# Optimization experiments

Hardware: AMD Instinct MI355X
Metric: run time of the kernel (lower is better)

## Reference

```python
import jax, jax.numpy as jnp
import numpy as np

B, S, D, H = 4, 2048, 1024, 16
HD = D // H
EPS = 1e-7  # K.epsilon()


def setup_inputs() -> dict:
    key = jax.random.key(0)
    ks = jax.random.split(key, 5)
    scale = 1.0 / np.sqrt(D)  # keep projections numerically tame (glorot-ish)
    return {
        "x": jax.random.normal(ks[0], (B, S, D), dtype=jnp.float32),
        "Wq": jax.random.normal(ks[1], (D, D), dtype=jnp.float32) * scale,
        "bq": jnp.zeros((D,), dtype=jnp.float32),
        "Wk": jax.random.normal(ks[2], (D, D), dtype=jnp.float32) * scale,
        "bk": jnp.zeros((D,), dtype=jnp.float32),
        "Wv": jax.random.normal(ks[3], (D, D), dtype=jnp.float32) * scale,
        "bv": jnp.zeros((D,), dtype=jnp.float32),
        "Wo": jax.random.normal(ks[4], (D, D), dtype=jnp.float32) * scale,
        "bo": jnp.zeros((D,), dtype=jnp.float32),
    }


def _split_heads(t):
    # [B,S,D] -> [B,H,S,HD]
    return t.reshape(B, S, H, HD).transpose(0, 2, 1, 3)


def reference(x, Wq, bq, Wk, bk, Wv, bv, Wo, bo):
    relu = jax.nn.relu
    # projections with post-activation (keras layer applies activation to each mapping)
    q = _split_heads(relu(x @ Wq + bq))
    k = _split_heads(relu(x @ Wk + bk))
    v = _split_heads(relu(x @ Wv + bv))
    # scaled dot-product scores, scale = sqrt(head_dim)
    e = jnp.einsum("bhqd,bhkd->bhqk", q, k) / jnp.sqrt(jnp.asarray(HD, x.dtype))
    # exp with row max over ALL keys (before masking), as in the source
    e = jnp.exp(e - jnp.max(e, axis=-1, keepdims=True))
    # history_only: multiplicative causal mask applied AFTER exp
    causal = (jnp.arange(S)[None, :] <= jnp.arange(S)[:, None]).astype(x.dtype)
    e = e * causal  # broadcasts over [B,H,S,S]
    a = e / (jnp.sum(e, axis=-1, keepdims=True) + EPS)
    ctx = jnp.einsum("bhqk,bhkd->bhqd", a, v)
    y = ctx.transpose(0, 2, 1, 3).reshape(B, S, D)  # merge heads
    return relu(y @ Wo + bo)
```

## Files before the change

kernel.cpp:

```cpp
#include <hip/hip_runtime.h>
#include <hip/hip_bf16.h>
#include <cstdint>
#include <cstddef>

#define B_  4
#define S_  2048
#define D_  1024
#define H_  16
#define HD_ 64

typedef _Float16 half8  __attribute__((ext_vector_type(8)));
typedef _Float16 half4v __attribute__((ext_vector_type(4)));
typedef float    f32x4  __attribute__((ext_vector_type(4)));

__device__ __forceinline__ void async_copy16(const void* g, void* l) {
    __builtin_amdgcn_global_load_lds(
        (const __attribute__((address_space(1))) unsigned int*)g,
        (__attribute__((address_space(3))) unsigned int*)l,
        16, 0, 0);
}

__device__ __forceinline__ half8 hscale8(half8 v, _Float16 s) {
    #pragma unroll
    for (int i = 0; i < 8; ++i) v[i] *= s;
    return v;
}


__global__ void cast_x_kernel(const float4* __restrict__ in, half4v* __restrict__ out, int n4) {
    int i = blockIdx.x * 256 + threadIdx.x;
    if (i < n4) {
        float4 v = in[i];
        half4v h = { (_Float16)v.x, (_Float16)v.y, (_Float16)v.z, (_Float16)v.w };
        out[i] = h;
    }
}

__global__ void transpose_cast4_kernel(
    const float* __restrict__ W0, const float* __restrict__ W1,
    const float* __restrict__ W2, const float* __restrict__ W3,
    _Float16* __restrict__ T0, _Float16* __restrict__ T1,
    _Float16* __restrict__ T2, _Float16* __restrict__ T3)
{
    __shared__ float tile[32][33];
    const float* Wsel[4] = { W0, W1, W2, W3 };
    _Float16*    Tsel[4] = { T0, T1, T2, T3 };
    const float* W  = Wsel[blockIdx.z];
    _Float16*    Wt = Tsel[blockIdx.z];
    const int bn = blockIdx.x * 32, bk = blockIdx.y * 32;
    const int tx = threadIdx.x, ty = threadIdx.y;
    #pragma unroll
    for (int i = 0; i < 32; i += 8)
        tile[ty + i][tx] = W[(size_t)(bk + ty + i) * D_ + bn + tx];
    __syncthreads();
    #pragma unroll
    for (int i = 0; i < 32; i += 8)
        Wt[(size_t)(bn + ty + i) * D_ + bk + tx] = (_Float16)tile[tx][ty + i];
}

template<int OUT_MODE>
__global__ __launch_bounds__(256, 2) void gemm_bt_kernel(
    const _Float16* __restrict__ A, const _Float16* __restrict__ Bt,
    const float* __restrict__ b0, const float* __restrict__ b1,
    const float* __restrict__ b2,
    void* __restrict__ C0, void* __restrict__ C1, void* __restrict__ C2,
    int M, int N, int K)
{
    __shared__ _Float16 As[128 * 64];
    __shared__ _Float16 Bs[128 * 64];
    const int tid  = threadIdx.x;
    const int wid  = tid >> 6, lane = tid & 63;
    const int lr   = lane & 15, lq = lane >> 4;
    const int m0   = blockIdx.x * 128, n0 = blockIdx.y * 128;
    const int wm   = (wid >> 1) * 64, wn = (wid & 1) * 64;
    const int srow = tid >> 3;
    const int csw  = ((tid & 7) ^ (srow & 7)) * 8;

    f32x4 acc[4][4] = {};

    for (int k0 = 0; k0 < K; k0 += 64) {
        __syncthreads();
        #pragma unroll
        for (int i = 0; i < 4; ++i) {
            async_copy16(A  + (size_t)(m0 + i * 32 + srow) * K + k0 + csw,
                         (char*)As + (i * 256 + wid * 64) * 16);
            async_copy16(Bt + (size_t)(n0 + i * 32 + srow) * K + k0 + csw,
                         (char*)Bs + (i * 256 + wid * 64) * 16);
        }
        __syncthreads();
        #pragma unroll
        for (int ks = 0; ks < 2; ++ks) {
            half8 af[4], bf[4];
            #pragma unroll
            for (int t = 0; t < 4; ++t) {
                af[t] = *(const half8*)(As + (wm + t * 16 + lr) * 64 + (((ks * 4 + lq) ^ (lr & 7)) * 8));
                bf[t] = *(const half8*)(Bs + (wn + t * 16 + lr) * 64 + (((ks * 4 + lq) ^ (lr & 7)) * 8));
            }
            #pragma unroll
            for (int mt = 0; mt < 4; ++mt)
                #pragma unroll
                for (int nt = 0; nt < 4; ++nt)
                    acc[mt][nt] = __builtin_amdgcn_mfma_f32_16x16x32_f16(
                        af[mt], bf[nt], acc[mt][nt], 0, 0, 0);
        }
    }

    const int seg = (OUT_MODE == 3) ? (n0 >> 10) : 0;
    const float* bp = (OUT_MODE == 3) ? (seg == 0 ? b0 : (seg == 1 ? b1 : b2)) : b0;

    #pragma unroll
    for (int mt = 0; mt < 4; ++mt) {
        const int row = m0 + wm + mt * 16 + lq * 4;
        #pragma unroll
        for (int nt = 0; nt < 4; ++nt) {
            const int col = n0 + wn + nt * 16 + lr;
            const int cl  = (OUT_MODE == 3) ? (col & 1023) : col;
            const float bb = bp[cl];
            if (OUT_MODE == 3 && seg == 2) {
                const int b = row >> 11, sq = row & 2047;
                const int h = cl >> 6, hd = cl & 63;
                half4v o;
                #pragma unroll
                for (int r = 0; r < 4; ++r) {
                    float v = acc[mt][nt][r] + bb;
                    o[r] = (_Float16)(v > 0.0f ? v : 0.0f);
                }
                *(half4v*)((_Float16*)C2 +
                           ((size_t)(b * 16 + h) * 64 + hd) * S_ + sq) = o;
            } else if (OUT_MODE == 3) {
                _Float16* dst = (_Float16*)(seg ? C1 : C0);
                #pragma unroll
                for (int r = 0; r < 4; ++r) {
                    float v = acc[mt][nt][r] + bb;
                    dst[(size_t)(row + r) * 1024 + cl] = (_Float16)(v > 0.0f ? v : 0.0f);
                }
            } else {
                #pragma unroll
                for (int r = 0; r < 4; ++r) {
                    float v = acc[mt][nt][r] + bb;
                    ((float*)C0)[(size_t)(row + r) * N + col] = v > 0.0f ? v : 0.0f;
                }
            }
        }
    }
}

__global__ __launch_bounds__(256, 4) void attn_kernel(
    const _Float16* __restrict__ Qg, const _Float16* __restrict__ Kg,
    const _Float16* __restrict__ Vtg, _Float16* __restrict__ Y)
{
    __shared__ _Float16 Ks[2][64 * 64];
    __shared__ _Float16 Vt[2][64 * 64];
    __shared__ _Float16 Ps[4][16 * 64];

    const int qt_lo = blockIdx.x;
    const int qt_hi = 31 - qt_lo;
    const int bh = blockIdx.y;
    const int b  = bh >> 4, h = bh & 15;
    const int tid = threadIdx.x, wid = tid >> 6, lane = tid & 63;
    const int lr = lane & 15, lq = lane >> 4;

    const size_t base  = ((size_t)b * S_) * D_ + (size_t)h * HD_;
    const _Float16* Vh = Vtg + (size_t)bh * 64 * S_;

    const int srow = tid >> 3;
    const int csw  = ((tid & 7) ^ (srow & 7)) * 8;

    const int qts[2] = { qt_lo, qt_hi };
    half8 aq[2][2];
    #pragma unroll
    for (int s = 0; s < 2; ++s) {
        const _Float16* qp = Qg + base + (size_t)(qts[s] * 64 + wid * 16 + lr) * D_;
        aq[s][0] = hscale8(*(const half8*)(qp + lq * 8),      (_Float16)0.18033688f);
        aq[s][1] = hscale8(*(const half8*)(qp + 32 + lq * 8), (_Float16)0.18033688f);
    }

    float lsum[2] = { 0.0f, 0.0f };
    f32x4 O[2][4] = {};

    auto issue_tile = [&](int kb) {
        const int bufi = kb & 1;
        #pragma unroll
        for (int i = 0; i < 2; ++i) {
            async_copy16(Kg + base + (size_t)(kb * 64 + i * 32 + srow) * D_ + csw,
                         (char*)Ks[bufi] + (i * 256 + wid * 64) * 16);
            async_copy16(Vh + (size_t)(i * 32 + srow) * S_ + kb * 64 + csw,
                         (char*)Vt[bufi] + (i * 256 + wid * 64) * 16);
        }
    };

    issue_tile(0);

    for (int kb = 0; kb <= qt_hi; ++kb) {
        const int cur = kb & 1;
        __syncthreads();
        if (kb < qt_hi) issue_tile(kb + 1);

        const _Float16* Kc = Ks[cur];
        const _Float16* Vc = Vt[cur];

        #pragma unroll
        for (int s = 0; s < 2; ++s) {
            if (s == 0 && kb > qt_lo) continue;

            f32x4 sc[4] = {};
            #pragma unroll
            for (int ks = 0; ks < 2; ++ks) {
                half8 kf[4];
                #pragma unroll
                for (int t = 0; t < 4; ++t)
                    kf[t] = *(const half8*)(Kc + (t * 16 + lr) * 64 + (((ks * 4 + lq) ^ (lr & 7)) * 8));
                #pragma unroll
                for (int t = 0; t < 4; ++t)
                    sc[t] = __builtin_amdgcn_mfma_f32_16x16x32_f16(kf[t], aq[s][ks], sc[t], 0, 0, 0);
            }

            const bool diag = (kb == qts[s]);
            const int qg = qts[s] * 64 + wid * 16 + lr;
            const int kbase = kb * 64 + lq * 4;
            float sum = 0.0f;
            _Float16* pw = Ps[wid];
            #pragma unroll
            for (int t = 0; t < 4; ++t) {
                half4v pv;
                #pragma unroll
                for (int r = 0; r < 4; ++r) {
                    float ev = __builtin_amdgcn_exp2f(fminf(sc[t][r] - 5.770780f, 15.8696f));
                    if (diag)
                        ev = (kbase + t * 16 + r <= qg) ? ev : 0.0f;
                    pv[r] = (_Float16)ev;
                    sum += ev;
                }
                *(half4v*)(pw + lr * 64 + (((t * 2 + (lq >> 1)) ^ (lr & 7)) * 8) + (lq & 1) * 4) = pv;
            }
            lsum[s] += sum;

            asm volatile("s_waitcnt lgkmcnt(0)" ::: "memory");

            #pragma unroll
            for (int ks = 0; ks < 2; ++ks) {
                half8 ap = *(const half8*)(pw + lr * 64 + (((ks * 4 + lq) ^ (lr & 7)) * 8));
                half8 bv[4];
                #pragma unroll
                for (int t = 0; t < 4; ++t)
                    bv[t] = *(const half8*)(Vc + (t * 16 + lr) * 64 + (((ks * 4 + lq) ^ (lr & 7)) * 8));
                #pragma unroll
                for (int t = 0; t < 4; ++t)
                    O[s][t] = __builtin_amdgcn_mfma_f32_16x16x32_f16(ap, bv[t], O[s][t], 0, 0, 0);
            }
        }
    }

    #pragma unroll
    for (int s = 0; s < 2; ++s) {
        float tot = lsum[s];
        tot += __shfl_xor(tot, 16);
        tot += __shfl_xor(tot, 32);
        const int q0 = qts[s] * 64 + wid * 16 + lq * 4;
        #pragma unroll
        for (int r = 0; r < 4; ++r) {
            const float inv = 1.0f / (__shfl(tot, lq * 4 + r) + 1e-7f);
            #pragma unroll
            for (int nt = 0; nt < 4; ++nt)
                Y[base + (size_t)(q0 + r) * D_ + nt * 16 + lr] = (_Float16)(O[s][nt][r] * inv);
        }
    }
}


extern "C" void kernel_launch(void* const* d_in, const int* in_sizes, int n_in,
                              void* d_out, int out_size, void* d_ws, size_t ws_size,
                              hipStream_t stream) {
    const float* x  = (const float*)d_in[0];
    const float* Wq = (const float*)d_in[1];
    const float* bq = (const float*)d_in[2];
    const float* Wk = (const float*)d_in[3];
    const float* bk = (const float*)d_in[4];
    const float* Wv = (const float*)d_in[5];
    const float* bv = (const float*)d_in[6];
    const float* Wo = (const float*)d_in[7];
    const float* bo = (const float*)d_in[8];

    char* ws = (char*)d_ws;
    _Float16* xh  = (_Float16*)ws;
    _Float16* wtq = (_Float16*)(ws + (size_t)16777216);
    _Float16* wtk = wtq + 1048576;
    _Float16* wtv = wtk + 1048576;
    _Float16* wto = wtv + 1048576;
    _Float16* Qh  = (_Float16*)(ws + (size_t)16777216 + 4 * (size_t)2097152);
    _Float16* Kh  = Qh + 8388608;
    _Float16* Vth = Kh + 8388608;
    _Float16* Yh  = Vth + 8388608;
    float* out = (float*)d_out;

    cast_x_kernel<<<8192, 256, 0, stream>>>((const float4*)x, (half4v*)xh, 2097152);
    transpose_cast4_kernel<<<dim3(32, 32, 4), dim3(32, 8), 0, stream>>>(
        Wq, Wk, Wv, Wo, wtq, wtk, wtv, wto);

    gemm_bt_kernel<3><<<dim3(64, 24), 256, 0, stream>>>(
        xh, wtq, bq, bk, bv, Qh, Kh, Vth, 8192, 3072, 1024);

    attn_kernel<<<dim3(16, 64), 256, 0, stream>>>(Qh, Kh, Vth, Yh);

    gemm_bt_kernel<0><<<dim3(64, 8), 256, 0, stream>>>(
        Yh, wto, bo, bo, bo, out, out, out, 8192, 1024, 1024);
}
```

Before: 271.4 us.

## Process four query tiles per attention block to reuse K/V fragments

Each attention workgroup now handles four 16-row query fragments per wave: two consecutive low tiles and two mirrored high tiles. K and V fragments are loaded from LDS once per key block and shared across all four query fragments, which cuts LDS traffic and global K/V reloads. The grid shrinks to 512 blocks with a remapped index to balance causal work, and launch bounds drop to 2 waves per SIMD. In exchange there are more registers and LDS per block and fewer blocks, which may hurt occupancy and latency hiding.

```diff
diff --git a/kernel.cpp b/kernel.cpp
--- a/kernel.cpp
+++ b/kernel.cpp
@@ -145,17 +145,17 @@
     }
 }
 
-__global__ __launch_bounds__(256, 4) void attn_kernel(
+__global__ __launch_bounds__(256, 2) void attn_kernel(
     const _Float16* __restrict__ Qg, const _Float16* __restrict__ Kg,
     const _Float16* __restrict__ Vtg, _Float16* __restrict__ Y)
 {
     __shared__ _Float16 Ks[2][64 * 64];
     __shared__ _Float16 Vt[2][64 * 64];
-    __shared__ _Float16 Ps[4][16 * 64];
-
-    const int qt_lo = blockIdx.x;
-    const int qt_hi = 31 - qt_lo;
-    const int bh = blockIdx.y;
+    __shared__ _Float16 Ps[4][4][16 * 64];
+
+    const int i  = blockIdx.x;
+    const int bh = ((i & 7) << 3) | (i >> 6);
+    const int p  = (i >> 3) & 7;
     const int b  = bh >> 4, h = bh & 15;
     const int tid = threadIdx.x, wid = tid >> 6, lane = tid & 63;
     const int lr = lane & 15, lq = lane >> 4;
@@ -166,60 +166,67 @@
     const int srow = tid >> 3;
     const int csw  = ((tid & 7) ^ (srow & 7)) * 8;
 
-    const int qts[2] = { qt_lo, qt_hi };
-    half8 aq[2][2];
-    #pragma unroll
-    for (int s = 0; s < 2; ++s) {
-        const _Float16* qp = Qg + base + (size_t)(qts[s] * 64 + wid * 16 + lr) * D_;
-        aq[s][0] = hscale8(*(const half8*)(qp + lq * 8),      (_Float16)0.18033688f);
-        aq[s][1] = hscale8(*(const half8*)(qp + 32 + lq * 8), (_Float16)0.18033688f);
-    }
-
-    float lsum[2] = { 0.0f, 0.0f };
-    f32x4 O[2][4] = {};
+    const int L = 128 * p, Hh = 1920 - 128 * p;
+    const int qb[4] = { L + 16 * wid, L + 64 + 16 * wid,
+                        Hh + 16 * wid, Hh + 64 + 16 * wid };
+    const int dk[4] = { 2 * p, 2 * p + 1, 30 - 2 * p, 31 - 2 * p };
+    const int nIter = 32 - 2 * p;
+
+    half8 aq[4][2];
+    #pragma unroll
+    for (int f = 0; f < 4; ++f) {
+        const _Float16* qp = Qg + base + (size_t)(qb[f] + lr) * D_;
+        aq[f][0] = hscale8(*(const half8*)(qp + lq * 8),      (_Float16)0.18033688f);
+        aq[f][1] = hscale8(*(const half8*)(qp + 32 + lq * 8), (_Float16)0.18033688f);
+    }
+
+    float lsum[4] = {};
+    f32x4 O[4][4] = {};
 
     auto issue_tile = [&](int kb) {
         const int bufi = kb & 1;
         #pragma unroll
-        for (int i = 0; i < 2; ++i) {
-            async_copy16(Kg + base + (size_t)(kb * 64 + i * 32 + srow) * D_ + csw,
-                         (char*)Ks[bufi] + (i * 256 + wid * 64) * 16);
-            async_copy16(Vh + (size_t)(i * 32 + srow) * S_ + kb * 64 + csw,
-                         (char*)Vt[bufi] + (i * 256 + wid * 64) * 16);
+        for (int ii = 0; ii < 2; ++ii) {
+            async_copy16(Kg + base + (size_t)(kb * 64 + ii * 32 + srow) * D_ + csw,
+                         (char*)Ks[bufi] + (ii * 256 + wid * 64) * 16);
+            async_copy16(Vh + (size_t)(ii * 32 + srow) * S_ + kb * 64 + csw,
+                         (char*)Vt[bufi] + (ii * 256 + wid * 64) * 16);
         }
     };
 
     issue_tile(0);
 
-    for (int kb = 0; kb <= qt_hi; ++kb) {
+    for (int kb = 0; kb < nIter; ++kb) {
         const int cur = kb & 1;
         __syncthreads();
-        if (kb < qt_hi) issue_tile(kb + 1);
+        if (kb + 1 < nIter) issue_tile(kb + 1);
 
         const _Float16* Kc = Ks[cur];
         const _Float16* Vc = Vt[cur];
 
-        #pragma unroll
-        for (int s = 0; s < 2; ++s) {
-            if (s == 0 && kb > qt_lo) continue;
+        half8 kf[2][4];
+        #pragma unroll
+        for (int ks = 0; ks < 2; ++ks)
+            #pragma unroll
+            for (int t = 0; t < 4; ++t)
+                kf[ks][t] = *(const half8*)(Kc + (t * 16 + lr) * 64 + (((ks * 4 + lq) ^ (lr & 7)) * 8));
+
+        #pragma unroll
+        for (int f = 0; f < 4; ++f) {
+            if (kb > dk[f]) continue;
 
             f32x4 sc[4] = {};
             #pragma unroll
-            for (int ks = 0; ks < 2; ++ks) {
-                half8 kf[4];
+            for (int ks = 0; ks < 2; ++ks)
                 #pragma unroll
                 for (int t = 0; t < 4; ++t)
-                    kf[t] = *(const half8*)(Kc + (t * 16 + lr) * 64 + (((ks * 4 + lq) ^ (lr & 7)) * 8));
-                #pragma unroll
-                for (int t = 0; t < 4; ++t)
-                    sc[t] = __builtin_amdgcn_mfma_f32_16x16x32_f16(kf[t], aq[s][ks], sc[t], 0, 0, 0);
-            }
-
-            const bool diag = (kb == qts[s]);
-            const int qg = qts[s] * 64 + wid * 16 + lr;
+                    sc[t] = __builtin_amdgcn_mfma_f32_16x16x32_f16(kf[ks][t], aq[f][ks], sc[t], 0, 0, 0);
+
+            const bool diag = (kb == dk[f]);
+            const int qg = qb[f] + lr;
             const int kbase = kb * 64 + lq * 4;
             float sum = 0.0f;
-            _Float16* pw = Ps[wid];
+            _Float16* pw = Ps[wid][f];
             #pragma unroll
             for (int t = 0; t < 4; ++t) {
                 half4v pv;
@@ -233,36 +240,44 @@
                 }
                 *(half4v*)(pw + lr * 64 + (((t * 2 + (lq >> 1)) ^ (lr & 7)) * 8) + (lq & 1) * 4) = pv;
             }
-            lsum[s] += sum;
-
-            asm volatile("s_waitcnt lgkmcnt(0)" ::: "memory");
-
+            lsum[f] += sum;
+        }
+
+        asm volatile("s_waitcnt lgkmcnt(0)" ::: "memory");
+
+        half8 bv[2][4];
+        #pragma unroll
+        for (int ks = 0; ks < 2; ++ks)
+            #pragma unroll
+            for (int t = 0; t < 4; ++t)
+                bv[ks][t] = *(const half8*)(Vc + (t * 16 + lr) * 64 + (((ks * 4 + lq) ^ (lr & 7)) * 8));
+
+        #pragma unroll
+        for (int f = 0; f < 4; ++f) {
+            if (kb > dk[f]) continue;
+            const _Float16* pw = Ps[wid][f];
             #pragma unroll
             for (int ks = 0; ks < 2; ++ks) {
                 half8 ap = *(const half8*)(pw + lr * 64 + (((ks * 4 + lq) ^ (lr & 7)) * 8));
-                half8 bv[4];
                 #pragma unroll
                 for (int t = 0; t < 4; ++t)
-                    bv[t] = *(const half8*)(Vc + (t * 16 + lr) * 64 + (((ks * 4 + lq) ^ (lr & 7)) * 8));
-                #pragma unroll
-                for (int t = 0; t < 4; ++t)
-                    O[s][t] = __builtin_amdgcn_mfma_f32_16x16x32_f16(ap, bv[t], O[s][t], 0, 0, 0);
+                    O[f][t] = __builtin_amdgcn_mfma_f32_16x16x32_f16(ap, bv[ks][t], O[f][t], 0, 0, 0);
             }
         }
     }
 
     #pragma unroll
-    for (int s = 0; s < 2; ++s) {
-        float tot = lsum[s];
+    for (int f = 0; f < 4; ++f) {
+        float tot = lsum[f];
         tot += __shfl_xor(tot, 16);
         tot += __shfl_xor(tot, 32);
-        const int q0 = qts[s] * 64 + wid * 16 + lq * 4;
+        const int q0 = qb[f] + lq * 4;
         #pragma unroll
         for (int r = 0; r < 4; ++r) {
             const float inv = 1.0f / (__shfl(tot, lq * 4 + r) + 1e-7f);
             #pragma unroll
             for (int nt = 0; nt < 4; ++nt)
-                Y[base + (size_t)(q0 + r) * D_ + nt * 16 + lr] = (_Float16)(O[s][nt][r] * inv);
+                Y[base + (size_t)(q0 + r) * D_ + nt * 16 + lr] = (_Float16)(O[f][nt][r] * inv);
         }
     }
 }
@@ -300,7 +315,7 @@
     gemm_bt_kernel<3><<<dim3(64, 24), 256, 0, stream>>>(
         xh, wtq, bq, bk, bv, Qh, Kh, Vth, 8192, 3072, 1024);
 
-    attn_kernel<<<dim3(16, 64), 256, 0, stream>>>(Qh, Kh, Vth, Yh);
+    attn_kernel<<<512, 256, 0, stream>>>(Qh, Kh, Vth, Yh);
 
     gemm_bt_kernel<0><<<dim3(64, 8), 256, 0, stream>>>(
         Yh, wto, bo, bo, bo, out, out, out, 8192, 1024, 1024);
```

Result: faster. 263.3 us (-3.0%).
